# Kernel tuning notes

Measured on AMD Instinct MI355X. Metric: run time of the kernel, lower is better.

Reference implementation:

```python
import jax, jax.numpy as jnp
import numpy as np

EMBED_DIM = 2048
NUM_HEADS = 16
HEAD_DIM = EMBED_DIM // NUM_HEADS
BATCH, SEQ = 4, 4096


def setup_inputs() -> dict:
    key = jax.random.key(0)
    k1, k2, k3, k4 = jax.random.split(key, 4)
    scale = 1.0 / np.sqrt(EMBED_DIM)
    x = jax.random.normal(k1, (BATCH, SEQ, EMBED_DIM), dtype=jnp.float32)
    W_qkv = jax.random.normal(k2, (EMBED_DIM, 3 * EMBED_DIM), dtype=jnp.float32) * scale
    W_out = jax.random.normal(k3, (EMBED_DIM, EMBED_DIM), dtype=jnp.float32) * scale
    b_out = jax.random.normal(k4, (EMBED_DIM,), dtype=jnp.float32) * 0.01
    return {"x": x, "W_qkv": W_qkv, "W_out": W_out, "b_out": b_out}


def reference(x, W_qkv, W_out, b_out):
    b, s, _ = x.shape
    # qkv: (b, s, 3, h, d)
    qkv = (x @ W_qkv).reshape(b, s, 3, NUM_HEADS, HEAD_DIM)
    q, k, v = qkv[:, :, 0], qkv[:, :, 1], qkv[:, :, 2]
    # NOTE: faithful to source — scores mix HEADS per token: (b, s, h, h)
    scores = jnp.einsum('bshd,bsHd->bshH', q, k) / jnp.sqrt(jnp.float32(HEAD_DIM))
    w = jax.nn.softmax(scores, axis=-1)
    attn = jnp.einsum('bshH,bsHd->bshd', w, v).reshape(b, s, EMBED_DIM)
    return attn @ W_out + b_out
```

## Files before the change

### kernel.cpp

```cpp
#include <hip/hip_runtime.h>
#include <hip/hip_bf16.h>
#include <cstdint>


#define TOKENS 16384
#define EMB    2048
#define NQKV   6144

typedef __bf16 bf16x8_t __attribute__((ext_vector_type(8)));
typedef float  f32x4_t  __attribute__((ext_vector_type(4)));

#define GLOAD16(gsrc, ldst)                                                    \
  __builtin_amdgcn_global_load_lds(                                            \
      (const __attribute__((address_space(1))) void*)(uintptr_t)(gsrc),        \
      (__attribute__((address_space(3))) void*)(uint32_t)(uintptr_t)(ldst),    \
      16, 0, 0)

static __device__ __forceinline__ unsigned short f32_to_bf16_bits(float f) {
  union { float f; uint32_t u; } x; x.f = f;
  uint32_t u = x.u;
  u += 0x7fffu + ((u >> 16) & 1u);
  return (unsigned short)(u >> 16);
}

__global__ __launch_bounds__(256) void cvt_f32_bf16(
    const float4* __restrict__ in, ushort4* __restrict__ out, int n4) {
  const int stride = gridDim.x * blockDim.x;
  for (int i = blockIdx.x * blockDim.x + threadIdx.x; i < n4; i += stride) {
    float4 v = in[i];
    ushort4 o;
    o.x = f32_to_bf16_bits(v.x);
    o.y = f32_to_bf16_bits(v.y);
    o.z = f32_to_bf16_bits(v.z);
    o.w = f32_to_bf16_bits(v.w);
    out[i] = o;
  }
}

__global__ __launch_bounds__(256) void transpose_cvt(
    const float* __restrict__ in, unsigned short* __restrict__ out, int R, int C) {
  __shared__ float tile[32][33];
  const int bx = blockIdx.x * 32;
  const int by = blockIdx.y * 32;
  const int tx = threadIdx.x;
  const int ty = threadIdx.y;
#pragma unroll
  for (int j = 0; j < 32; j += 8)
    tile[ty + j][tx] = in[(size_t)(by + ty + j) * C + bx + tx];
  __syncthreads();
#pragma unroll
  for (int j = 0; j < 32; j += 8)
    out[(size_t)(bx + ty + j) * R + by + tx] = f32_to_bf16_bits(tile[tx][ty + j]);
}

template <bool OUT_BF16>
__global__ __launch_bounds__(512, 1) void gemm_bt(
    const unsigned short* __restrict__ A,
    const unsigned short* __restrict__ BT,
    unsigned short* __restrict__ Cb,
    float* __restrict__ Cf,
    const float* __restrict__ bias,
    int M, int N) {
  constexpr int K = 2048;
  constexpr int BK = 64;
  constexpr int NKT = K / BK;
  __shared__ __align__(16) char lds[131072];

  const int nbx = N / 256;
  const int nwg = gridDim.x;
  const int bid = blockIdx.x;
  const int swzb = (bid & 7) * (nwg >> 3) + (bid >> 3);
  const int by = swzb / nbx;
  const int bx = swzb % nbx;

  const int t    = threadIdx.x;
  const int lane = t & 63;
  const int wid  = t >> 6;
  const int wr   = wid >> 2;
  const int wc   = wid & 3;
  const int lr   = lane & 15;
  const int g    = lane >> 4;

  const unsigned short* aSrc = A  + (size_t)by * 256 * K;
  const unsigned short* bSrc = BT + (size_t)bx * 256 * K;

  int aoff[2], boff[2];
#pragma unroll
  for (int i = 0; i < 2; ++i) {
    const int p   = (i * 512 + t) * 16;
    const int lo  = p ^ (((p >> 7) & 7) << 4);
    const int rih = lo >> 7;
    const int kbe = (lo & 127) >> 1;
    aoff[i] = (((rih >> 6) << 7) + (rih & 63)) * K + kbe;
    boff[i] = (((rih >> 5) << 6) + (rih & 31)) * K + kbe;
  }
  const int ldst = wid << 10;

  auto stageA = [&](int h, int k0, char* bufA) {
#pragma unroll
    for (int i = 0; i < 2; ++i)
      GLOAD16(aSrc + aoff[i] + h * (64 * K) + k0, bufA + h * 16384 + i * 8192 + ldst);
  };
  auto stageB = [&](int h, int k0, char* bufB) {
#pragma unroll
    for (int i = 0; i < 2; ++i)
      GLOAD16(bSrc + boff[i] + h * (32 * K) + k0, bufB + h * 16384 + i * 8192 + ldst);
  };

  const int sw   = (lr & 7) << 4;
  const int col0 = (g * 16) ^ sw;
  const int col1 = (64 + g * 16) ^ sw;
  const int aRow = (wr * 64 + lr) * 128;
  const int bRow = (wc * 32 + lr) * 128;

  f32x4_t acc[8][4] = {};
  bf16x8_t av0[4][2], av1[4][2];
  bf16x8_t bv0[2][2], bv1[2][2];

#define LDA_INTO(dst, bufA_, q)                                                \
  {                                                                            \
    const char* _b = (bufA_) + (q) * 16384 + aRow;                             \
    _Pragma("unroll") for (int m2 = 0; m2 < 4; ++m2) {                         \
      dst[m2][0] = *(const bf16x8_t*)(_b + m2 * 2048 + col0);                  \
      dst[m2][1] = *(const bf16x8_t*)(_b + m2 * 2048 + col1);                  \
    }                                                                          \
  }
#define LDB_INTO(dst, bufB_, pair)                                             \
  {                                                                            \
    _Pragma("unroll") for (int e = 0; e < 2; ++e) {                            \
      const int nf = (pair) * 2 + e;                                           \
      const char* _b = (bufB_) + (nf >> 1) * 16384 + (nf & 1) * 2048 + bRow;   \
      dst[e][0] = *(const bf16x8_t*)(_b + col0);                               \
      dst[e][1] = *(const bf16x8_t*)(_b + col1);                               \
    }                                                                          \
  }
#define MFMAQ(AV, BV, Q, PAIR)                                                 \
  _Pragma("unroll") for (int m2 = 0; m2 < 4; ++m2)                             \
  _Pragma("unroll") for (int e = 0; e < 2; ++e)                                \
  _Pragma("unroll") for (int ks = 0; ks < 2; ++ks)                             \
    acc[(Q) * 4 + m2][(PAIR) * 2 + e] = __builtin_amdgcn_mfma_f32_16x16x32_bf16( \
        AV[m2][ks], BV[e][ks], acc[(Q) * 4 + m2][(PAIR) * 2 + e], 0, 0, 0);

#define SBR __builtin_amdgcn_sched_barrier(0)
#define TAIL(NN)                                                               \
  SBR; __builtin_amdgcn_s_barrier();                                           \
  asm volatile("s_waitcnt lgkmcnt(" #NN ")" ::: "memory");                     \
  SBR; __builtin_amdgcn_s_setprio(1);
#define PEND                                                                   \
  __builtin_amdgcn_s_setprio(0); SBR; __builtin_amdgcn_s_barrier();

  {
    char* b0A = lds;
    char* b0B = lds + 32768;
    char* b1A = lds + 65536;
    char* b1B = b1A + 32768;
    stageA(0, 0, b0A); stageA(1, 0, b0A);
    stageB(0, 0, b0B); stageB(1, 0, b0B);
    stageA(0, BK, b1A);
    stageB(1, BK, b1B);
    asm volatile("s_waitcnt vmcnt(4)" ::: "memory");
    __builtin_amdgcn_s_barrier();
    LDA_INTO(av0, b0A, 0);
    LDB_INTO(bv0, b0B, 0);
    SBR;
  }

  for (int kt = 0; kt < NKT; ++kt) {
    char* cA = lds + (kt & 1) * 65536;
    char* cB = cA + 32768;
    char* nA = lds + ((kt + 1) & 1) * 65536;
    char* nB = nA + 32768;
    const int k1 = (kt + 1) * BK;
    const int k2 = (kt + 2) * BK;
    const bool s1 = kt + 1 < NKT;
    const bool s2 = kt + 2 < NKT;

    if (s1) stageA(1, k1, nA);
    TAIL(0);
    MFMAQ(av0, bv0, 0, 0);
    LDB_INTO(bv1, cB, 1);
    PEND;

    LDA_INTO(av1, cA, 1);
    SBR;
    if (s1) stageB(0, k1, nB);
    TAIL(8); MFMAQ(av0, bv1, 0, 1); PEND;

    if (s2) stageA(0, k2, cA);
    TAIL(0); MFMAQ(av1, bv1, 1, 1); PEND;

    if (s2) stageB(1, k2, cB);
    if (s2) { asm volatile("s_waitcnt vmcnt(4)" ::: "memory"); }
    else    { asm volatile("s_waitcnt vmcnt(0)" ::: "memory"); }
    SBR;
    if (s1) {
      LDA_INTO(av0, nA, 0);
      TAIL(8);
    } else {
      TAIL(0);
    }
    MFMAQ(av1, bv0, 1, 0);
    if (s1) { LDB_INTO(bv0, nB, 0); }
    PEND;
  }

  const int rbase = by * 256 + wr * 128 + g * 4;
  const int cbase = bx * 256 + wc * 64 + lr;
#pragma unroll
  for (int m = 0; m < 8; ++m) {
#pragma unroll
    for (int nf = 0; nf < 4; ++nf) {
      const int col = cbase + nf * 16;
#pragma unroll
      for (int j = 0; j < 4; ++j) {
        const size_t off = (size_t)(rbase + (m >> 2) * 64 + (m & 3) * 16 + j) * N + col;
        if constexpr (OUT_BF16) {
          Cb[off] = f32_to_bf16_bits(acc[m][nf][j]);
        } else {
          Cf[off] = acc[m][nf][j] + bias[col];
        }
      }
    }
  }
#undef LDA_INTO
#undef LDB_INTO
#undef MFMAQ
#undef SBR
#undef TAIL
#undef PEND
}

__global__ __launch_bounds__(256) void attn_heads(
    const unsigned short* __restrict__ qkv,
    unsigned short* __restrict__ attn) {
  __shared__ __align__(16) unsigned short sQKV[NQKV];
  __shared__ float sW[16][16];

  const int t = threadIdx.x;
  const size_t qbase = (size_t)blockIdx.x * NQKV;

  const uint4* gp = (const uint4*)(qkv + qbase);
  uint4* l = (uint4*)sQKV;
#pragma unroll
  for (int i = 0; i < 3; ++i) {
    const int idx = i * 256 + t;
    int dst = idx;
    if (idx >= 256 && idx < 512) {
      const int r = (idx - 256) >> 4;
      const int c = idx & 15;
      dst = 256 + r * 16 + (c ^ (r & 7));
    }
    l[dst] = gp[idx];
  }
  __syncthreads();

  const int h = t >> 4;
  const int H = t & 15;
  const bf16x8_t* q8 = (const bf16x8_t*)sQKV + h * 16;
  const bf16x8_t* k8 = (const bf16x8_t*)sQKV + 256;
  float s = 0.f;
#pragma unroll
  for (int d8 = 0; d8 < 16; ++d8) {
    bf16x8_t qv = q8[d8];
    bf16x8_t kv = k8[H * 16 + (d8 ^ (H & 7))];
#pragma unroll
    for (int j = 0; j < 8; ++j)
      s = fmaf((float)qv[j], (float)kv[j], s);
  }
  s *= 0.08838834764831843f;

  float mx = s;
#pragma unroll
  for (int o = 8; o; o >>= 1) mx = fmaxf(mx, __shfl_xor(mx, o));
  const float e = __expf(s - mx);
  float sum = e;
#pragma unroll
  for (int o = 8; o; o >>= 1) sum += __shfl_xor(sum, o);
  sW[h][H] = e / sum;
  __syncthreads();

  const int d0c = t & 15;
  const bf16x8_t* v8 = (const bf16x8_t*)sQKV + 512;
  float accv[8] = {};
#pragma unroll
  for (int j = 0; j < 16; ++j) {
    const float w = sW[h][j];
    const bf16x8_t vv = v8[j * 16 + d0c];
#pragma unroll
    for (int jj = 0; jj < 8; ++jj)
      accv[jj] = fmaf(w, (float)vv[jj], accv[jj]);
  }
  bf16x8_t o;
#pragma unroll
  for (int jj = 0; jj < 8; ++jj) o[jj] = (__bf16)accv[jj];
  *(bf16x8_t*)(attn + (size_t)blockIdx.x * EMB + h * 128 + d0c * 8) = o;
}

extern "C" void kernel_launch(void* const* d_in, const int* in_sizes, int n_in,
                              void* d_out, int out_size, void* d_ws, size_t ws_size,
                              hipStream_t stream) {
  const float* x    = (const float*)d_in[0];
  const float* Wqkv = (const float*)d_in[1];
  const float* Wout = (const float*)d_in[2];
  const float* bout = (const float*)d_in[3];
  float* out = (float*)d_out;

  unsigned short* xb    = (unsigned short*)d_ws;
  unsigned short* wqkvT = xb    + (size_t)33554432;
  unsigned short* woutT = wqkvT + (size_t)12582912;
  unsigned short* qkv   = woutT + (size_t)4194304;
  unsigned short* attn  = qkv   + (size_t)100663296;

  cvt_f32_bf16<<<2048, 256, 0, stream>>>((const float4*)x, (ushort4*)xb, 33554432 / 4);
  transpose_cvt<<<dim3(6144 / 32, 2048 / 32), dim3(32, 8), 0, stream>>>(Wqkv, wqkvT, 2048, 6144);
  transpose_cvt<<<dim3(2048 / 32, 2048 / 32), dim3(32, 8), 0, stream>>>(Wout, woutT, 2048, 2048);
  gemm_bt<true><<<(16384 / 256) * (6144 / 256), 512, 0, stream>>>(
      xb, wqkvT, qkv, nullptr, nullptr, 16384, 6144);
  attn_heads<<<TOKENS, 256, 0, stream>>>(qkv, attn);
  gemm_bt<false><<<(16384 / 256) * (2048 / 256), 512, 0, stream>>>(
      attn, woutT, nullptr, out, bout, 16384, 2048);
}
```

Before: 644.0 us.

## Restructure GEMM main loop with deeper prefetch and peeled tail iterations

Rewrites the K-loop of the bf16 GEMM kernel. The prologue now stages a full second K-tile, and each iteration prefetches tile k+2 in quarters, interleaved between MFMA phases, with fine-grained vmcnt waits. The last two iterations are peeled into specialized bodies, which removes runtime s1/s2 branches and fixes the waitcnt values. This is meant to hide global-to-LDS load latency better and cut barrier stalls, at the cost of more complex wait accounting and a risk of LDS race bugs.

Result: faster. 627.8 us (-2.5%).

```diff
diff --git a/kernel.cpp b/kernel.cpp
--- a/kernel.cpp
+++ b/kernel.cpp
@@ -148,6 +148,41 @@
   SBR; __builtin_amdgcn_s_setprio(1);
 #define PEND                                                                   \
   __builtin_amdgcn_s_setprio(0); SBR; __builtin_amdgcn_s_barrier();
+#define VMC(NN) asm volatile("s_waitcnt vmcnt(" #NN ")" ::: "memory"); SBR;
+
+#define BODY(KT, S1, S2, VM3, VM4, T4)                                         \
+  {                                                                            \
+    char* cA = lds + ((KT) & 1) * 65536;                                       \
+    char* cB = cA + 32768;                                                     \
+    char* nA = lds + (((KT) + 1) & 1) * 65536;                                 \
+    char* nB = nA + 32768;                                                     \
+    const int k2 = ((KT) + 2) * BK;                                            \
+      \
+    LDB_INTO(bv1, cB, 1); SBR;                                                 \
+    TAIL(4);                                                                   \
+    MFMAQ(av0, bv0, 0, 0);                                                     \
+    LDA_INTO(av1, cA, 1);                                                      \
+    PEND;                                                                      \
+                               \
+    if (S2) { stageA(0, k2, cA); } SBR;                                        \
+    TAIL(8);                                                                   \
+    MFMAQ(av0, bv1, 0, 1);                                                     \
+    PEND;                                                                      \
+                                         \
+    VMC(VM3);                                                                  \
+    if (S2) { stageB(0, k2, cB); } SBR;                                        \
+    TAIL(0);                                                                   \
+    MFMAQ(av1, bv1, 1, 1);                                                     \
+    PEND;                                                                      \
+                             \
+    VMC(VM4);                                                                  \
+    if (S2) { stageA(1, k2, cA); stageB(1, k2, cB); } SBR;                     \
+    if (S1) { LDA_INTO(av0, nA, 0); } SBR;                                     \
+    TAIL(T4);                                                                  \
+    MFMAQ(av1, bv0, 1, 0);                                                     \
+    if (S1) { LDB_INTO(bv0, nB, 0); }                                          \
+    PEND;                                                                      \
+  }
 
   {
     char* b0A = lds;
@@ -157,52 +192,21 @@
     stageA(0, 0, b0A); stageA(1, 0, b0A);
     stageB(0, 0, b0B); stageB(1, 0, b0B);
     stageA(0, BK, b1A);
+    stageB(0, BK, b1B);
+    stageA(1, BK, b1A);
     stageB(1, BK, b1B);
-    asm volatile("s_waitcnt vmcnt(4)" ::: "memory");
+    asm volatile("s_waitcnt vmcnt(8)" ::: "memory");
     __builtin_amdgcn_s_barrier();
     LDA_INTO(av0, b0A, 0);
     LDB_INTO(bv0, b0B, 0);
     SBR;
   }
 
-  for (int kt = 0; kt < NKT; ++kt) {
-    char* cA = lds + (kt & 1) * 65536;
-    char* cB = cA + 32768;
-    char* nA = lds + ((kt + 1) & 1) * 65536;
-    char* nB = nA + 32768;
-    const int k1 = (kt + 1) * BK;
-    const int k2 = (kt + 2) * BK;
-    const bool s1 = kt + 1 < NKT;
-    const bool s2 = kt + 2 < NKT;
-
-    if (s1) stageA(1, k1, nA);
-    TAIL(0);
-    MFMAQ(av0, bv0, 0, 0);
-    LDB_INTO(bv1, cB, 1);
-    PEND;
-
-    LDA_INTO(av1, cA, 1);
-    SBR;
-    if (s1) stageB(0, k1, nB);
-    TAIL(8); MFMAQ(av0, bv1, 0, 1); PEND;
-
-    if (s2) stageA(0, k2, cA);
-    TAIL(0); MFMAQ(av1, bv1, 1, 1); PEND;
-
-    if (s2) stageB(1, k2, cB);
-    if (s2) { asm volatile("s_waitcnt vmcnt(4)" ::: "memory"); }
-    else    { asm volatile("s_waitcnt vmcnt(0)" ::: "memory"); }
-    SBR;
-    if (s1) {
-      LDA_INTO(av0, nA, 0);
-      TAIL(8);
-    } else {
-      TAIL(0);
-    }
-    MFMAQ(av1, bv0, 1, 0);
-    if (s1) { LDB_INTO(bv0, nB, 0); }
-    PEND;
-  }
+  for (int kt = 0; kt < NKT - 2; ++kt) {
+    BODY(kt, 1, 1, 6, 4, 8);
+  }
+  BODY(NKT - 2, 1, 0, 4, 0, 8);
+  BODY(NKT - 1, 0, 0, 0, 0, 0);
 
   const int rbase = by * 256 + wr * 128 + g * 4;
   const int cbase = bx * 256 + wc * 64 + lr;
@@ -228,6 +232,8 @@
 #undef SBR
 #undef TAIL
 #undef PEND
+#undef VMC
+#undef BODY
 }
 
 __global__ __launch_bounds__(256) void attn_heads(
```
